# Kernel optimization log

Hardware: AMD Instinct MI355X
Metric: run time of the kernel (lower is better)

## Reference

```python
import jax, jax.numpy as jnp
import numpy as np

B, N, F_IN, OUT_FEATS, NUM_CLS, NUM_INDS = 256, 200, 200, 256, 8, 512
PCT_EDGES = 20
K = int(PCT_EDGES / 100 * N * (N - 1) / 2)  # 3980 hard edges
TAU = 1.0


def setup_inputs() -> dict:
    key = jax.random.key(0)
    ks = jax.random.split(key, 6)
    x = jax.random.normal(ks[0], (B, N, F_IN), dtype=jnp.float32)
    gumbel_u = jax.random.uniform(ks[1], (B, N, N), dtype=jnp.float32)
    nets = jax.random.normal(ks[2], (NUM_INDS, N, N), dtype=jnp.float32)
    w_gnn = jax.random.normal(ks[3], (F_IN, OUT_FEATS), dtype=jnp.float32) / np.sqrt(F_IN).astype(np.float32)
    w_lin = jax.random.normal(ks[4], (OUT_FEATS, NUM_CLS), dtype=jnp.float32) / np.sqrt(OUT_FEATS).astype(np.float32)
    b_lin = jnp.zeros((NUM_CLS,), dtype=jnp.float32)
    net_index = jax.random.randint(ks[5], (B,), 0, NUM_INDS)
    return {"x": x, "gumbel_u": gumbel_u, "nets": nets, "w_gnn": w_gnn,
            "w_lin": w_lin, "b_lin": b_lin, "net_index": net_index}


def _gumbel_softkmax(logits, u, k, tau):
    # logits: [B, N, N]; u: uniform(0,1) noise -> Gumbel(0,1) via -log(-log(u))
    b, n, _ = logits.shape
    g = -jnp.log(-jnp.log(jnp.clip(u, 1e-10, 1.0 - 1e-10)))
    g = (logits + g) / tau
    sym = (g + jnp.swapaxes(g, 1, 2)) * 0.5                      # symmetrize
    y_soft = jax.nn.softmax(sym.reshape(b, -1), axis=-1).reshape(b, n, n)
    upper_flat = jnp.triu(y_soft).reshape(b, -1)                 # upper tri incl. diag
    _, idx = jax.lax.top_k(upper_flat, k)                        # [B, k]
    y_hard = jnp.zeros_like(upper_flat).at[jnp.arange(b)[:, None], idx].set(1.0)
    y_hard = y_hard.reshape(b, n, n)
    diag = jnp.diagonal(y_hard, axis1=-2, axis2=-1)              # [B, N]
    eye = jnp.eye(n, dtype=y_hard.dtype)
    y_hard = y_hard + jnp.swapaxes(y_hard, 1, 2) - diag[:, :, None] * eye
    # straight-through estimator
    return y_hard - jax.lax.stop_gradient(y_soft) + y_soft


def reference(x, gumbel_u, nets, w_gnn, w_lin, b_lin, net_index):
    selected = nets[net_index]                                   # [B, N, N]
    adj = _gumbel_softkmax(selected, gumbel_u, K, TAU)
    # gnn: relu(adj @ x @ W_gnn)  -> embeddings [B, N, OUT_FEATS]
    emb = jax.nn.relu(jnp.einsum('bij,bjf,fo->bio', adj, x, w_gnn))
    out = emb @ w_lin + b_lin                                    # [B, N, NUM_CLS]
    return out, emb, adj
```

## Files before the change

### kernel.cpp

```cpp
#include <hip/hip_runtime.h>
#include <math.h>

#define B_SZ 256
#define N_SZ 200
#define NN (N_SZ * N_SZ)
#define FIN 200
#define OUT_F 256
#define NCLS 8
#define KSEL 3980
#define NUPPER 20100
#define KSTRIDE 20128
#define NT 7
#define NTILES 28

#define KGRP_PB 25
#define XWM_PB (KGRP_PB * 2048)
#define MROW_W 8
#define MG_PB (N_SZ * MROW_W)

#define EMB_OFF (B_SZ * N_SZ * NCLS)
#define ADJ_OFF (EMB_OFF + B_SZ * N_SZ * OUT_F)

#define KEYS_OFF_B   0
#define WKG_OFF_B    26214400
#define MG_OFF_B     26329088

typedef unsigned short ushort_t;
typedef float f32x4 __attribute__((ext_vector_type(4)));
typedef short bf16x8 __attribute__((ext_vector_type(8)));

__device__ __forceinline__ unsigned sortkey(float f) {
    unsigned u = __float_as_uint(f);
    return (u & 0x80000000u) ? ~u : (u | 0x80000000u);
}

__device__ __forceinline__ ushort_t f2b(float f) {
    unsigned u = __float_as_uint(f);
    return (ushort_t)((u + 0x7FFFu + ((u >> 16) & 1u)) >> 16);
}

__device__ __forceinline__ bf16x8 f2b8(float4 lo, float4 hi) {
    bf16x8 r;
    r[0] = (short)f2b(lo.x); r[1] = (short)f2b(lo.y);
    r[2] = (short)f2b(lo.z); r[3] = (short)f2b(lo.w);
    r[4] = (short)f2b(hi.x); r[5] = (short)f2b(hi.y);
    r[6] = (short)f2b(hi.z); r[7] = (short)f2b(hi.w);
    return r;
}

__device__ __forceinline__ void tile_decode(int t, int& ti, int& tj) {
    int a = 0, rem = t;
    while (rem >= NT - a) { rem -= NT - a; ++a; }
    ti = a; tj = a + rem;
}

__device__ __forceinline__ int rowbase(int i) {
    return i * N_SZ - (i * (i - 1)) / 2;
}

__global__ __launch_bounds__(256) void kA(
    const float* __restrict__ gu, const float* __restrict__ nets,
    const int* __restrict__ net_index, unsigned* __restrict__ keys,
    const float* __restrict__ wg, ushort_t* __restrict__ wkg)
{
    const int blk = blockIdx.x;
    if (blk >= B_SZ * NTILES) {
        int pb = blk - B_SZ * NTILES;
        int e = pb * 256 + threadIdx.x;
        int kg = e >> 11;
        int rem = e & 2047;
        int n = rem >> 3;
        int ki = rem & 7;
        int k = kg * 8 + ki;
        wkg[e] = (k < FIN) ? f2b(wg[k * OUT_F + n]) : (ushort_t)0;
        return;
    }
    const int b = blk / NTILES;
    int ti, tj; tile_decode(blk % NTILES, ti, tj);
    const int i0 = ti * 32, j0 = tj * 32;
    const float* ub = gu + (size_t)b * NN;
    const float* lb = nets + (size_t)net_index[b] * NN;

    __shared__ float Hij[32][33];
    __shared__ float Hji[32][33];

    const int r = threadIdx.x >> 5;
    const int c = threadIdx.x & 31;

    #pragma unroll
    for (int s = 0; s < 4; ++s) {
        int rr = r + 8 * s;
        int i = i0 + rr, j = j0 + c;
        if (i < N_SZ && j < N_SZ) {
            float u = ub[i * N_SZ + j];
            u = fminf(fmaxf(u, 1e-10f), 1.0f - 1e-10f);
            Hij[rr][c] = lb[i * N_SZ + j] - logf(-logf(u));
        }
        if (ti != tj) {
            int i2 = j0 + rr, j2 = i0 + c;
            if (i2 < N_SZ && j2 < N_SZ) {
                float u = ub[i2 * N_SZ + j2];
                u = fminf(fmaxf(u, 1e-10f), 1.0f - 1e-10f);
                Hji[rr][c] = lb[i2 * N_SZ + j2] - logf(-logf(u));
            }
        }
    }
    __syncthreads();

    unsigned* kb = keys + (size_t)b * KSTRIDE;
    #pragma unroll
    for (int s = 0; s < 4; ++s) {
        int rr = r + 8 * s;
        int i = i0 + rr, j = j0 + c;
        if (i < N_SZ && j < N_SZ && i <= j) {
            float hji = (ti == tj) ? Hij[c][rr] : Hji[c][rr];
            float sv = 0.5f * ((Hij[rr][c]) + hji);
            int base = i * N_SZ - (i * (i - 1)) / 2;
            kb[base + (j - i)] = sortkey(sv);
        }
    }
}

__global__ __launch_bounds__(1024) void kSelW(
    const unsigned* __restrict__ keys, float* __restrict__ out_base,
    unsigned* __restrict__ Mg)
{
    const int b = blockIdx.x;
    const int tid = threadIdx.x;
    const int lane = tid & 63;
    const int wv = tid >> 6;
    __shared__ __align__(16) unsigned kl[NUPPER];
    __shared__ unsigned hist16[16][256];
    __shared__ unsigned hist[256];
    __shared__ unsigned wtot[16];
    __shared__ unsigned M[N_SZ][7];
    __shared__ unsigned sPrefix;
    __shared__ int sKK;

    {
        const int4* kb4 = (const int4*)(keys + (size_t)b * KSTRIDE);
        int4* kl4 = (int4*)kl;
        for (int q = tid; q < 5025; q += 1024) kl4[q] = kb4[q];
    }
    for (int q = tid; q < N_SZ * 7; q += 1024) ((unsigned*)M)[q] = 0;

    unsigned prefix = 0;
    int kk = KSEL;
    for (int round = 0; round < 4; ++round) {
        const int shift = 24 - 8 * round;
        unsigned own = 0, v = 0;
        if (round == 0) {
            for (int q = tid; q < 16 * 256; q += 1024) ((unsigned*)hist16)[q] = 0;
            __syncthreads();
            for (int idx = tid; idx < NUPPER; idx += 1024)
                atomicAdd(&hist16[wv][kl[idx] >> 24], 1u);
            __syncthreads();
            if (tid < 256) {
                #pragma unroll
                for (int q = 0; q < 16; ++q) own += hist16[q][tid];
            }
        } else {
            if (tid < 256) hist[tid] = 0;
            __syncthreads();
            for (int idx = tid; idx < NUPPER; idx += 1024) {
                unsigned key = kl[idx];
                if ((key >> (shift + 8)) == prefix)
                    atomicAdd(&hist[(key >> shift) & 255u], 1u);
            }
            __syncthreads();
            if (tid < 256) own = hist[tid];
        }
        if (tid < 256) {
            v = own;
            #pragma unroll
            for (int off = 1; off < 64; off <<= 1) {
                unsigned t = __shfl_down(v, off, 64);
                if (lane + off < 64) v += t;
            }
            if (lane == 0) wtot[wv] = v;
        }
        __syncthreads();
        if (tid < 256) {
            unsigned add = 0;
            #pragma unroll
            for (int q = 1; q < 4; ++q) if (wv + q < 4) add += wtot[wv + q];
            unsigned sfxv = v + add;
            unsigned above = sfxv - own;
            if (sfxv >= (unsigned)kk && above < (unsigned)kk) {
                sPrefix = (prefix << 8) | (unsigned)tid;
                sKK = kk - (int)above;
            }
        }
        __syncthreads();
        prefix = sPrefix;
        kk = sKK;
    }
    const unsigned kth = prefix;

    const int lo = tid * 20;
    const int hi = (lo + 20 < NUPPER) ? lo + 20 : NUPPER;
    unsigned mycnt = 0;
    for (int idx = lo; idx < hi; ++idx)
        if (kl[idx] == kth) ++mycnt;
    unsigned v = mycnt;
    #pragma unroll
    for (int off = 1; off < 64; off <<= 1) {
        unsigned t = __shfl_up(v, off, 64);
        if (lane >= off) v += t;
    }
    if (lane == 63) wtot[wv] = v;
    __syncthreads();
    unsigned addp = 0;
    for (int q = 0; q < wv; ++q) addp += wtot[q];
    unsigned rank = v + addp - mycnt;

    if (lo < NUPPER) {
        int iLo = 0, iHi = N_SZ - 1;
        while (iLo < iHi) {
            int mid = (iLo + iHi + 1) >> 1;
            if (rowbase(mid) <= lo) iLo = mid; else iHi = mid - 1;
        }
        int i = iLo;
        int nextBase = rowbase(i + 1);
        for (int idx = lo; idx < hi; ++idx) {
            while (idx >= nextBase) { ++i; nextBase = rowbase(i + 1); }
            unsigned key = kl[idx];
            bool dec;
            if (key > kth) dec = true;
            else if (key == kth) { dec = (rank < (unsigned)kk); ++rank; }
            else dec = false;
            if (dec) {
                int j = i + (idx - rowbase(i));
                atomicOr(&M[i][j >> 5], 1u << (j & 31));
                atomicOr(&M[j][i >> 5], 1u << (i & 31));
            }
        }
    }
    __syncthreads();

    float* adj = out_base + ADJ_OFF + (size_t)b * NN;
    for (int e = tid; e < 10000; e += 1024) {
        int i = e / 50;
        int j0 = (e % 50) * 4;
        unsigned wbits = M[i][j0 >> 5] >> (j0 & 31);
        float4 v4;
        v4.x = (wbits & 1u) ? 1.0f : 0.0f;
        v4.y = (wbits & 2u) ? 1.0f : 0.0f;
        v4.z = (wbits & 4u) ? 1.0f : 0.0f;
        v4.w = (wbits & 8u) ? 1.0f : 0.0f;
        *(float4*)(adj + (size_t)i * N_SZ + j0) = v4;
    }
    unsigned* mb = Mg + (size_t)b * MG_PB;
    for (int e = tid; e < MG_PB; e += 1024) {
        int i = e >> 3, ww = e & 7;
        mb[e] = (ww < 7) ? M[i][ww] : 0u;
    }
}

__global__ __launch_bounds__(256) void k2_mfma(
    const float* __restrict__ x, const ushort_t* __restrict__ wkg,
    ushort_t* __restrict__ xwm)
{
    const int r0 = blockIdx.x * 32;
    const int tid = threadIdx.x;
    const int w = tid >> 6;
    const int l = tid & 63;
    const int g = l >> 4;
    const int r = l & 15;

    __shared__ __align__(16) ushort_t Cs[32 * 256];

    f32x4 acc[2][4];
    #pragma unroll
    for (int mf = 0; mf < 2; ++mf)
        #pragma unroll
        for (int nf = 0; nf < 4; ++nf)
            acc[mf][nf] = (f32x4){0.f, 0.f, 0.f, 0.f};

    for (int c = 0; c < 7; ++c) {
        const int koff = (c * 32 + g * 8 < FIN) ? (c * 32 + g * 8) : 0;
        bf16x8 af[2], bf[4];
        #pragma unroll
        for (int mf = 0; mf < 2; ++mf) {
            const float* ap = x + (size_t)(r0 + mf * 16 + r) * FIN + koff;
            float4 lo = *(const float4*)ap;
            float4 hi = *(const float4*)(ap + 4);
            af[mf] = f2b8(lo, hi);
        }
        #pragma unroll
        for (int nf = 0; nf < 4; ++nf)
            bf[nf] = *(const bf16x8*)(wkg + c * 8192 + g * 2048 + (w * 64 + nf * 16 + r) * 8);
        #pragma unroll
        for (int mf = 0; mf < 2; ++mf)
            #pragma unroll
            for (int nf = 0; nf < 4; ++nf)
                acc[mf][nf] = __builtin_amdgcn_mfma_f32_16x16x32_bf16(
                    af[mf], bf[nf], acc[mf][nf], 0, 0, 0);
    }

    #pragma unroll
    for (int mf = 0; mf < 2; ++mf) {
        #pragma unroll
        for (int jj = 0; jj < 4; ++jj) {
            int row = mf * 16 + g * 4 + jj;
            #pragma unroll
            for (int nf = 0; nf < 4; ++nf) {
                int col = w * 64 + nf * 16 + r;
                Cs[((row >> 3) << 11) + col * 8 + (row & 7)] = f2b(acc[mf][nf][jj]);
            }
        }
    }
    __syncthreads();
    #pragma unroll
    for (int kg = 0; kg < 4; ++kg) {
        int grow0 = r0 + kg * 8;
        int bb = grow0 / N_SZ;
        int jb = grow0 % N_SZ;
        ushort_t* dst = xwm + (size_t)bb * XWM_PB + ((jb >> 3) << 11);
        *(int4*)(dst + tid * 8) = *(const int4*)(Cs + (kg << 11) + tid * 8);
    }
}

__global__ __launch_bounds__(256) void k3_fused(
    const unsigned* __restrict__ Mg, const ushort_t* __restrict__ xwm,
    const float* __restrict__ wl, const float* __restrict__ bl,
    float* __restrict__ out_base)
{
    const int blk = blockIdx.x;
    const int xcd = blk & 7;
    const int idx = blk >> 3;
    const int b = xcd + 8 * (idx / 13);
    const int mt = idx % 13;
    const int tid = threadIdx.x;
    const int w = tid >> 6;
    const int l = tid & 63;
    const int g = l >> 4;
    const int r = l & 15;

    const ushort_t* xwb = xwm + (size_t)b * XWM_PB;

    __shared__ __align__(16) float Es[16 * 256];
    float (*red)[4][4][8] = (float(*)[4][4][8])Es;

    int arow = mt * 16 + r; if (arow > N_SZ - 1) arow = N_SZ - 1;
    const int4* mrow = (const int4*)(Mg + (size_t)b * MG_PB + arow * MROW_W);
    int4 m0 = mrow[0];
    int4 m1 = mrow[1];
    unsigned wds[8];
    wds[0] = (unsigned)m0.x; wds[1] = (unsigned)m0.y;
    wds[2] = (unsigned)m0.z; wds[3] = (unsigned)m0.w;
    wds[4] = (unsigned)m1.x; wds[5] = (unsigned)m1.y;
    wds[6] = (unsigned)m1.z; wds[7] = (unsigned)m1.w;

    f32x4 acc[4];
    #pragma unroll
    for (int nf = 0; nf < 4; ++nf) acc[nf] = (f32x4){0.f, 0.f, 0.f, 0.f};

    #pragma unroll
    for (int c = 0; c < 7; ++c) {
        unsigned bits = (wds[c] >> (g * 8)) & 0xFFu;
        int dw[4];
        #pragma unroll
        for (int q = 0; q < 4; ++q)
            dw[q] = ((bits >> (2 * q)) & 1u ? 0x3F80 : 0)
                  | ((bits >> (2 * q + 1)) & 1u ? 0x3F800000 : 0);
        int4 ai = {dw[0], dw[1], dw[2], dw[3]};
        bf16x8 af = *(bf16x8*)&ai;

        bf16x8 bf[4];
        #pragma unroll
        for (int nf = 0; nf < 4; ++nf)
            bf[nf] = *(const bf16x8*)(xwb + c * 8192 + g * 2048 + (w * 64 + nf * 16 + r) * 8);
        #pragma unroll
        for (int nf = 0; nf < 4; ++nf)
            acc[nf] = __builtin_amdgcn_mfma_f32_16x16x32_bf16(
                af, bf[nf], acc[nf], 0, 0, 0);
    }

    #pragma unroll
    for (int j = 0; j < 4; ++j) {
        int rowl = g * 4 + j;
        #pragma unroll
        for (int nf = 0; nf < 4; ++nf)
            Es[rowl * 256 + w * 64 + nf * 16 + r] = fmaxf(acc[nf][j], 0.0f);
    }
    __syncthreads();
    #pragma unroll
    for (int q = 0; q < 4; ++q) {
        int e = q * 256 + tid;
        int rowl = e >> 6;
        int c4 = e & 63;
        int grow = mt * 16 + rowl;
        if (grow < N_SZ) {
            float4 v = *(const float4*)(Es + rowl * 256 + c4 * 4);
            *(float4*)(out_base + EMB_OFF + ((size_t)b * N_SZ + grow) * OUT_F + c4 * 4) = v;
        }
    }
    __syncthreads();

    float wlv[4][NCLS];
    #pragma unroll
    for (int nf = 0; nf < 4; ++nf) {
        int col = w * 64 + nf * 16 + r;
        #pragma unroll
        for (int cls = 0; cls < NCLS; ++cls) wlv[nf][cls] = wl[col * NCLS + cls];
    }
    #pragma unroll
    for (int j = 0; j < 4; ++j) {
        float e0 = fmaxf(acc[0][j], 0.0f);
        float e1 = fmaxf(acc[1][j], 0.0f);
        float e2 = fmaxf(acc[2][j], 0.0f);
        float e3 = fmaxf(acc[3][j], 0.0f);
        float pr[NCLS];
        #pragma unroll
        for (int cls = 0; cls < NCLS; ++cls)
            pr[cls] = e0 * wlv[0][cls] + e1 * wlv[1][cls]
                    + e2 * wlv[2][cls] + e3 * wlv[3][cls];
        #pragma unroll
        for (int off = 1; off <= 8; off <<= 1) {
            #pragma unroll
            for (int cls = 0; cls < NCLS; ++cls)
                pr[cls] += __shfl_xor(pr[cls], off, 64);
        }
        if (r < NCLS) red[w][g][j][r] = pr[r];
    }
    __syncthreads();

    if (tid < 16 * NCLS) {
        int rowl = tid >> 3, cls = tid & 7;
        int gg = rowl >> 2, jj = rowl & 3;
        int grow = mt * 16 + rowl;
        if (grow < N_SZ) {
            float s = red[0][gg][jj][cls] + red[1][gg][jj][cls]
                    + red[2][gg][jj][cls] + red[3][gg][jj][cls] + bl[cls];
            out_base[((size_t)b * N_SZ + grow) * NCLS + cls] = s;
        }
    }
}

extern "C" void kernel_launch(void* const* d_in, const int* in_sizes, int n_in,
                              void* d_out, int out_size, void* d_ws, size_t ws_size,
                              hipStream_t stream) {
    const float* x    = (const float*)d_in[0];
    const float* gu   = (const float*)d_in[1];
    const float* nets = (const float*)d_in[2];
    const float* wg   = (const float*)d_in[3];
    const float* wl   = (const float*)d_in[4];
    const float* bl   = (const float*)d_in[5];
    const int*   nidx = (const int*)d_in[6];
    float* out = (float*)d_out;

    char* ws = (char*)d_ws;
    unsigned* keys    = (unsigned*)(ws + KEYS_OFF_B);
    ushort_t* xwm     = (ushort_t*)(ws + KEYS_OFF_B);
    ushort_t* wkg     = (ushort_t*)(ws + WKG_OFF_B);
    unsigned* Mg      = (unsigned*)(ws + MG_OFF_B);

    kA<<<B_SZ * NTILES + 224, 256, 0, stream>>>(gu, nets, nidx, keys, wg, wkg);
    kSelW<<<B_SZ, 1024, 0, stream>>>(keys, out, Mg);
    k2_mfma<<<(B_SZ * N_SZ) / 32, 256, 0, stream>>>(x, wkg, xwm);
    k3_fused<<<B_SZ * 13, 256, 0, stream>>>(Mg, xwm, wl, bl, out);
}
```

Before: 127.6 us.

## Merge top-k select and x@W GEMM into one launch with 16-bit radix prefilter

Combines the per-batch top-k selection kernel and the x·W_gnn MFMA kernel into a single launch: the first 256 blocks do selection and the remaining blocks each run four 32-row GEMM tiles, writing bf16 results straight to global memory instead of staging them through shared memory. Selection now radix-sorts only the upper 16 key bits held in LDS as ushorts, gathers the keys that tie on that prefix into a capped candidate list, and finishes the last two radix rounds on that list. Tie ranking is done by an O(C^2) scan. The goal is to cut one launch, halve LDS traffic, and overlap selection with the GEMM. The risks are candidate-list overflow past 2048 and a slow tie loop, and xwm moves to its own workspace region so it no longer aliases keys.

```diff
diff --git a/kernel.cpp b/kernel.cpp
--- a/kernel.cpp
+++ b/kernel.cpp
@@ -12,6 +12,7 @@
 #define KSTRIDE 20128
 #define NT 7
 #define NTILES 28
+#define CAND_CAP 2048
 
 #define KGRP_PB 25
 #define XWM_PB (KGRP_PB * 2048)
@@ -22,12 +23,14 @@
 #define ADJ_OFF (EMB_OFF + B_SZ * N_SZ * OUT_F)
 
 #define KEYS_OFF_B   0
-#define WKG_OFF_B    26214400
-#define MG_OFF_B     26329088
+#define WKG_OFF_B    20611072
+#define MG_OFF_B     20725760
+#define XWM_OFF_B    22364160
 
 typedef unsigned short ushort_t;
 typedef float f32x4 __attribute__((ext_vector_type(4)));
 typedef short bf16x8 __attribute__((ext_vector_type(8)));
+typedef ushort_t u16x4 __attribute__((ext_vector_type(4)));
 
 __device__ __forceinline__ unsigned sortkey(float f) {
     unsigned u = __float_as_uint(f);
@@ -121,61 +124,122 @@
     }
 }
 
-__global__ __launch_bounds__(1024) void kSelW(
-    const unsigned* __restrict__ keys, float* __restrict__ out_base,
-    unsigned* __restrict__ Mg)
+__global__ __launch_bounds__(1024) void kSW2(
+    const unsigned* __restrict__ keys, const float* __restrict__ x,
+    const ushort_t* __restrict__ wkg, float* __restrict__ out_base,
+    unsigned* __restrict__ Mg, ushort_t* __restrict__ xwm)
 {
-    const int b = blockIdx.x;
+    const int blk = blockIdx.x;
     const int tid = threadIdx.x;
-    const int lane = tid & 63;
-    const int wv = tid >> 6;
-    __shared__ __align__(16) unsigned kl[NUPPER];
-    __shared__ unsigned hist16[16][256];
+
+    __shared__ __align__(16) ushort_t k16[NUPPER];
     __shared__ unsigned hist[256];
     __shared__ unsigned wtot[16];
     __shared__ unsigned M[N_SZ][7];
+    __shared__ unsigned candIdx[CAND_CAP];
+    __shared__ unsigned candKey[CAND_CAP];
     __shared__ unsigned sPrefix;
     __shared__ int sKK;
+    __shared__ unsigned sCnt;
+
+    if (blk >= B_SZ) {
+        const int grp = tid >> 8;
+        const int t = tid & 255;
+        const int w = t >> 6;
+        const int l = t & 63;
+        const int g = l >> 4;
+        const int r = l & 15;
+        const int r0 = (blk - B_SZ) * 128 + grp * 32;
+
+        f32x4 acc[2][4];
+        #pragma unroll
+        for (int mf = 0; mf < 2; ++mf)
+            #pragma unroll
+            for (int nf = 0; nf < 4; ++nf)
+                acc[mf][nf] = (f32x4){0.f, 0.f, 0.f, 0.f};
+
+        for (int c = 0; c < 7; ++c) {
+            const int koff = (c * 32 + g * 8 < FIN) ? (c * 32 + g * 8) : 0;
+            bf16x8 af[2], bf[4];
+            #pragma unroll
+            for (int mf = 0; mf < 2; ++mf) {
+                const float* ap = x + (size_t)(r0 + mf * 16 + r) * FIN + koff;
+                float4 lo = *(const float4*)ap;
+                float4 hi = *(const float4*)(ap + 4);
+                af[mf] = f2b8(lo, hi);
+            }
+            #pragma unroll
+            for (int nf = 0; nf < 4; ++nf)
+                bf[nf] = *(const bf16x8*)(wkg + c * 8192 + g * 2048 + (w * 64 + nf * 16 + r) * 8);
+            #pragma unroll
+            for (int mf = 0; mf < 2; ++mf)
+                #pragma unroll
+                for (int nf = 0; nf < 4; ++nf)
+                    acc[mf][nf] = __builtin_amdgcn_mfma_f32_16x16x32_bf16(
+                        af[mf], bf[nf], acc[mf][nf], 0, 0, 0);
+        }
+
+        #pragma unroll
+        for (int mf = 0; mf < 2; ++mf) {
+            int kgl = 2 * mf + (g >> 1);
+            int grow0 = r0 + kgl * 8;
+            int bb = grow0 / N_SZ;
+            int jb = grow0 % N_SZ;
+            size_t base = (size_t)bb * XWM_PB + ((size_t)(jb >> 3) << 11) + (g & 1) * 4;
+            #pragma unroll
+            for (int nf = 0; nf < 4; ++nf) {
+                int col = w * 64 + nf * 16 + r;
+                u16x4 pv;
+                pv[0] = f2b(acc[mf][nf][0]);
+                pv[1] = f2b(acc[mf][nf][1]);
+                pv[2] = f2b(acc[mf][nf][2]);
+                pv[3] = f2b(acc[mf][nf][3]);
+                *(u16x4*)(xwm + base + col * 8) = pv;
+            }
+        }
+        return;
+    }
+
+    const int b = blk;
+    const int lane = tid & 63;
+    const int wv = tid >> 6;
+    const unsigned* kb = keys + (size_t)b * KSTRIDE;
 
     {
-        const int4* kb4 = (const int4*)(keys + (size_t)b * KSTRIDE);
-        int4* kl4 = (int4*)kl;
-        for (int q = tid; q < 5025; q += 1024) kl4[q] = kb4[q];
+        const int4* kb4 = (const int4*)kb;
+        for (int q = tid; q < 5025; q += 1024) {
+            int4 kv = kb4[q];
+            u16x4 h;
+            h[0] = (ushort_t)((unsigned)kv.x >> 16);
+            h[1] = (ushort_t)((unsigned)kv.y >> 16);
+            h[2] = (ushort_t)((unsigned)kv.z >> 16);
+            h[3] = (ushort_t)((unsigned)kv.w >> 16);
+            *(u16x4*)(k16 + 4 * q) = h;
+        }
     }
     for (int q = tid; q < N_SZ * 7; q += 1024) ((unsigned*)M)[q] = 0;
-
-    unsigned prefix = 0;
+    if (tid == 0) sCnt = 0;
+
+    unsigned pfx = 0;
     int kk = KSEL;
-    for (int round = 0; round < 4; ++round) {
-        const int shift = 24 - 8 * round;
+    for (int round = 0; round < 2; ++round) {
+        const int shift = 8 - 8 * round;
+        if (tid < 256) hist[tid] = 0;
+        __syncthreads();
+        for (int idx = tid; idx < NUPPER; idx += 1024) {
+            unsigned kv = k16[idx];
+            bool in = (round == 0) || ((kv >> 8) == pfx);
+            if (in) atomicAdd(&hist[(kv >> shift) & 255u], 1u);
+        }
+        __syncthreads();
         unsigned own = 0, v = 0;
-        if (round == 0) {
-            for (int q = tid; q < 16 * 256; q += 1024) ((unsigned*)hist16)[q] = 0;
-            __syncthreads();
-            for (int idx = tid; idx < NUPPER; idx += 1024)
-                atomicAdd(&hist16[wv][kl[idx] >> 24], 1u);
-            __syncthreads();
-            if (tid < 256) {
-                #pragma unroll
-                for (int q = 0; q < 16; ++q) own += hist16[q][tid];
-            }
-        } else {
-            if (tid < 256) hist[tid] = 0;
-            __syncthreads();
-            for (int idx = tid; idx < NUPPER; idx += 1024) {
-                unsigned key = kl[idx];
-                if ((key >> (shift + 8)) == prefix)
-                    atomicAdd(&hist[(key >> shift) & 255u], 1u);
-            }
-            __syncthreads();
-            if (tid < 256) own = hist[tid];
-        }
         if (tid < 256) {
+            own = hist[tid];
             v = own;
             #pragma unroll
             for (int off = 1; off < 64; off <<= 1) {
-                unsigned t = __shfl_down(v, off, 64);
-                if (lane + off < 64) v += t;
+                unsigned tt = __shfl_down(v, off, 64);
+                if (lane + off < 64) v += tt;
             }
             if (lane == 0) wtot[wv] = v;
         }
@@ -187,53 +251,108 @@
             unsigned sfxv = v + add;
             unsigned above = sfxv - own;
             if (sfxv >= (unsigned)kk && above < (unsigned)kk) {
-                sPrefix = (prefix << 8) | (unsigned)tid;
+                sPrefix = (pfx << 8) | (unsigned)tid;
                 sKK = kk - (int)above;
             }
         }
         __syncthreads();
-        prefix = sPrefix;
+        pfx = sPrefix;
         kk = sKK;
     }
-    const unsigned kth = prefix;
-
-    const int lo = tid * 20;
-    const int hi = (lo + 20 < NUPPER) ? lo + 20 : NUPPER;
-    unsigned mycnt = 0;
-    for (int idx = lo; idx < hi; ++idx)
-        if (kl[idx] == kth) ++mycnt;
-    unsigned v = mycnt;
-    #pragma unroll
-    for (int off = 1; off < 64; off <<= 1) {
-        unsigned t = __shfl_up(v, off, 64);
-        if (lane >= off) v += t;
-    }
-    if (lane == 63) wtot[wv] = v;
-    __syncthreads();
-    unsigned addp = 0;
-    for (int q = 0; q < wv; ++q) addp += wtot[q];
-    unsigned rank = v + addp - mycnt;
-
-    if (lo < NUPPER) {
-        int iLo = 0, iHi = N_SZ - 1;
-        while (iLo < iHi) {
-            int mid = (iLo + iHi + 1) >> 1;
-            if (rowbase(mid) <= lo) iLo = mid; else iHi = mid - 1;
-        }
-        int i = iLo;
-        int nextBase = rowbase(i + 1);
-        for (int idx = lo; idx < hi; ++idx) {
-            while (idx >= nextBase) { ++i; nextBase = rowbase(i + 1); }
-            unsigned key = kl[idx];
-            bool dec;
-            if (key > kth) dec = true;
-            else if (key == kth) { dec = (rank < (unsigned)kk); ++rank; }
-            else dec = false;
-            if (dec) {
-                int j = i + (idx - rowbase(i));
-                atomicOr(&M[i][j >> 5], 1u << (j & 31));
-                atomicOr(&M[j][i >> 5], 1u << (i & 31));
-            }
+    const unsigned P16 = pfx;
+
+    __syncthreads();
+    for (int idx = tid; idx < NUPPER; idx += 1024) {
+        if ((unsigned)k16[idx] == P16) {
+            unsigned p = atomicAdd(&sCnt, 1u);
+            if (p < CAND_CAP) { candIdx[p] = (unsigned)idx; candKey[p] = kb[idx]; }
+        }
+    }
+    __syncthreads();
+    int C = (int)sCnt; if (C > CAND_CAP) C = CAND_CAP;
+
+    unsigned pfx32 = P16;
+    for (int round = 0; round < 2; ++round) {
+        const int shift = 8 - 8 * round;
+        if (tid < 256) hist[tid] = 0;
+        __syncthreads();
+        for (int q = tid; q < C; q += 1024) {
+            unsigned key = candKey[q];
+            if ((key >> (shift + 8)) == pfx32)
+                atomicAdd(&hist[(key >> shift) & 255u], 1u);
+        }
+        __syncthreads();
+        unsigned own = 0, v = 0;
+        if (tid < 256) {
+            own = hist[tid];
+            v = own;
+            #pragma unroll
+            for (int off = 1; off < 64; off <<= 1) {
+                unsigned tt = __shfl_down(v, off, 64);
+                if (lane + off < 64) v += tt;
+            }
+            if (lane == 0) wtot[wv] = v;
+        }
+        __syncthreads();
+        if (tid < 256) {
+            unsigned add = 0;
+            #pragma unroll
+            for (int q = 1; q < 4; ++q) if (wv + q < 4) add += wtot[wv + q];
+            unsigned sfxv = v + add;
+            unsigned above = sfxv - own;
+            if (sfxv >= (unsigned)kk && above < (unsigned)kk) {
+                sPrefix = (pfx32 << 8) | (unsigned)tid;
+                sKK = kk - (int)above;
+            }
+        }
+        __syncthreads();
+        pfx32 = sPrefix;
+        kk = sKK;
+    }
+    const unsigned kth32 = pfx32;
+    const int kkf = kk;
+
+    {
+        const int lo = tid * 20;
+        const int hi = (lo + 20 < NUPPER) ? lo + 20 : NUPPER;
+        if (lo < NUPPER) {
+            int iLo = 0, iHi = N_SZ - 1;
+            while (iLo < iHi) {
+                int mid = (iLo + iHi + 1) >> 1;
+                if (rowbase(mid) <= lo) iLo = mid; else iHi = mid - 1;
+            }
+            int i = iLo;
+            int nextBase = rowbase(i + 1);
+            for (int idx = lo; idx < hi; ++idx) {
+                while (idx >= nextBase) { ++i; nextBase = rowbase(i + 1); }
+                if ((unsigned)k16[idx] > P16) {
+                    int j = i + (idx - rowbase(i));
+                    atomicOr(&M[i][j >> 5], 1u << (j & 31));
+                    atomicOr(&M[j][i >> 5], 1u << (i & 31));
+                }
+            }
+        }
+    }
+    for (int q = tid; q < C; q += 1024) {
+        unsigned key = candKey[q];
+        bool dec = false;
+        if (key > kth32) dec = true;
+        else if (key == kth32) {
+            int rank = 0;
+            for (int p = 0; p < C; ++p)
+                if (candKey[p] == kth32 && candIdx[p] < candIdx[q]) ++rank;
+            dec = (rank < kkf);
+        }
+        if (dec) {
+            int idx = (int)candIdx[q];
+            int iLo = 0, iHi = N_SZ - 1;
+            while (iLo < iHi) {
+                int mid = (iLo + iHi + 1) >> 1;
+                if (rowbase(mid) <= idx) iLo = mid; else iHi = mid - 1;
+            }
+            int i = iLo, j = i + (idx - rowbase(i));
+            atomicOr(&M[i][j >> 5], 1u << (j & 31));
+            atomicOr(&M[j][i >> 5], 1u << (i & 31));
         }
     }
     __syncthreads();
@@ -254,70 +373,6 @@
     for (int e = tid; e < MG_PB; e += 1024) {
         int i = e >> 3, ww = e & 7;
         mb[e] = (ww < 7) ? M[i][ww] : 0u;
-    }
-}
-
-__global__ __launch_bounds__(256) void k2_mfma(
-    const float* __restrict__ x, const ushort_t* __restrict__ wkg,
-    ushort_t* __restrict__ xwm)
-{
-    const int r0 = blockIdx.x * 32;
-    const int tid = threadIdx.x;
-    const int w = tid >> 6;
-    const int l = tid & 63;
-    const int g = l >> 4;
-    const int r = l & 15;
-
-    __shared__ __align__(16) ushort_t Cs[32 * 256];
-
-    f32x4 acc[2][4];
-    #pragma unroll
-    for (int mf = 0; mf < 2; ++mf)
-        #pragma unroll
-        for (int nf = 0; nf < 4; ++nf)
-            acc[mf][nf] = (f32x4){0.f, 0.f, 0.f, 0.f};
-
-    for (int c = 0; c < 7; ++c) {
-        const int koff = (c * 32 + g * 8 < FIN) ? (c * 32 + g * 8) : 0;
-        bf16x8 af[2], bf[4];
-        #pragma unroll
-        for (int mf = 0; mf < 2; ++mf) {
-            const float* ap = x + (size_t)(r0 + mf * 16 + r) * FIN + koff;
-            float4 lo = *(const float4*)ap;
-            float4 hi = *(const float4*)(ap + 4);
-            af[mf] = f2b8(lo, hi);
-        }
-        #pragma unroll
-        for (int nf = 0; nf < 4; ++nf)
-            bf[nf] = *(const bf16x8*)(wkg + c * 8192 + g * 2048 + (w * 64 + nf * 16 + r) * 8);
-        #pragma unroll
-        for (int mf = 0; mf < 2; ++mf)
-            #pragma unroll
-            for (int nf = 0; nf < 4; ++nf)
-                acc[mf][nf] = __builtin_amdgcn_mfma_f32_16x16x32_bf16(
-                    af[mf], bf[nf], acc[mf][nf], 0, 0, 0);
-    }
-
-    #pragma unroll
-    for (int mf = 0; mf < 2; ++mf) {
-        #pragma unroll
-        for (int jj = 0; jj < 4; ++jj) {
-            int row = mf * 16 + g * 4 + jj;
-            #pragma unroll
-            for (int nf = 0; nf < 4; ++nf) {
-                int col = w * 64 + nf * 16 + r;
-                Cs[((row >> 3) << 11) + col * 8 + (row & 7)] = f2b(acc[mf][nf][jj]);
-            }
-        }
-    }
-    __syncthreads();
-    #pragma unroll
-    for (int kg = 0; kg < 4; ++kg) {
-        int grow0 = r0 + kg * 8;
-        int bb = grow0 / N_SZ;
-        int jb = grow0 % N_SZ;
-        ushort_t* dst = xwm + (size_t)bb * XWM_PB + ((jb >> 3) << 11);
-        *(int4*)(dst + tid * 8) = *(const int4*)(Cs + (kg << 11) + tid * 8);
     }
 }
 
@@ -452,12 +507,11 @@
 
     char* ws = (char*)d_ws;
     unsigned* keys    = (unsigned*)(ws + KEYS_OFF_B);
-    ushort_t* xwm     = (ushort_t*)(ws + KEYS_OFF_B);
     ushort_t* wkg     = (ushort_t*)(ws + WKG_OFF_B);
     unsigned* Mg      = (unsigned*)(ws + MG_OFF_B);
+    ushort_t* xwm     = (ushort_t*)(ws + XWM_OFF_B);
 
     kA<<<B_SZ * NTILES + 224, 256, 0, stream>>>(gu, nets, nidx, keys, wg, wkg);
-    kSelW<<<B_SZ, 1024, 0, stream>>>(keys, out, Mg);
-    k2_mfma<<<(B_SZ * N_SZ) / 32, 256, 0, stream>>>(x, wkg, xwm);
+    kSW2<<<B_SZ + 400, 1024, 0, stream>>>(keys, x, wkg, out, Mg, xwm);
     k3_fused<<<B_SZ * 13, 256, 0, stream>>>(Mg, xwm, wl, bl, out);
 }
```

New measurement: 133.7 us. 4.8% more time.
